# Optimization experiments

Hardware: AMD Instinct MI355X
Metric: run time of the kernel (lower is better)

The kernel has to match this reference:

```python
import jax, jax.numpy as jnp
import numpy as np

N = 50000
E = 1600000
IN_DIM = 128
H = 8
D = 16  # out_dim per head


def setup_inputs() -> dict:
    key = jax.random.key(0)
    ks = jax.random.split(key, 9)
    h = jax.random.normal(ks[0], (N, IN_DIM), dtype=jnp.float32)
    src = jax.random.randint(ks[1], (E,), 0, N, dtype=jnp.int32)
    dst = jax.random.randint(ks[2], (E,), 0, N, dtype=jnp.int32)
    s = 1.0 / np.sqrt(IN_DIM)
    WQ = jax.random.uniform(ks[3], (IN_DIM, H * D), jnp.float32, -s, s)
    WK = jax.random.uniform(ks[4], (IN_DIM, H * D), jnp.float32, -s, s)
    WV = jax.random.uniform(ks[5], (IN_DIM, H * D), jnp.float32, -s, s)
    bQ = jax.random.uniform(ks[6], (H * D,), jnp.float32, -s, s)
    bK = jax.random.uniform(ks[7], (H * D,), jnp.float32, -s, s)
    bV = jax.random.uniform(ks[8], (H * D,), jnp.float32, -s, s)
    return {"h": h, "src": src, "dst": dst, "WQ": WQ, "WK": WK, "WV": WV,
            "bQ": bQ, "bK": bK, "bV": bV}


def reference(h, src, dst, WQ, WK, WV, bQ, bK, bV):
    # Node projections -> [N, H, D]
    Q = (h @ WQ + bQ).reshape(-1, H, D)
    K = (h @ WK + bK).reshape(-1, H, D)
    V = (h @ WV + bV).reshape(-1, H, D)
    # Edge scores: dot(K[src], Q[dst]) per head, scaled+clamped exp -> [E, H]
    scale = jnp.float32(np.sqrt(D))
    score = jnp.exp(jnp.clip(jnp.sum(K[src] * Q[dst], axis=-1) / scale, -5.0, 5.0))
    # Scatter-sum to destination nodes
    wV = jax.ops.segment_sum(score[:, :, None] * V[src], dst, num_segments=N)  # [N, H, D]
    z = jax.ops.segment_sum(score, dst, num_segments=N)  # [N, H]
    return wV / z[:, :, None]
```

## Files before the change

kernel.cpp:

```cpp
#include <hip/hip_runtime.h>

#define N_NODES 50000
#define N_PAD   50048
#define N_EDGES 1600000
#define HD 128
#define CHUNK 4096
#define NCHUNK ((N_EDGES + CHUNK - 1) / CHUNK)
#define NBUCKET ((N_NODES + 127) / 128)

typedef __attribute__((ext_vector_type(8))) short short8;
typedef __attribute__((ext_vector_type(4))) float floatx4;

union U4S8 { uint4 u; short8 s; };

__device__ __forceinline__ unsigned short f2bf(float f) {
    unsigned u = __float_as_uint(f);
    unsigned r = (u + 0x7fffu + ((u >> 16) & 1u)) >> 16;
    return (unsigned short)r;
}

__global__ __launch_bounds__(256) void k_chunkhist(
    const int* __restrict__ dst, int* __restrict__ chunkhist, int* __restrict__ btot,
    const float* __restrict__ WQ, const float* __restrict__ WK, const float* __restrict__ WV,
    unsigned short* __restrict__ Wf) {
    int t = threadIdx.x, c = blockIdx.x;
    if (c >= NCHUNK) {
        int tid = (c - NCHUNK) * 256 + t;
        int lane = tid & 63;
        int kstep = (tid >> 6) & 3;
        int ntile = tid >> 8;
        int g = ntile >> 3;
        int col = (ntile & 7) * 16 + (lane & 15);
        int k0 = kstep * 32 + (lane >> 4) * 8;
        const float* W = (g == 0) ? WQ : (g == 1) ? WK : WV;
        unsigned short r[8];
#pragma unroll
        for (int j = 0; j < 8; ++j)
            r[j] = f2bf(W[(size_t)(k0 + j) * HD + col]);
        *(uint4*)(Wf + (size_t)tid * 8) = *(uint4*)r;
        return;
    }
    __shared__ int hist[NBUCKET];
    for (int i = t; i < NBUCKET; i += 256) hist[i] = 0;
    __syncthreads();
    int e0 = c * CHUNK;
    int cnt = min(CHUNK, N_EDGES - e0);
    const uint4* d4 = (const uint4*)(dst + e0);
    int cnt4 = cnt >> 2;
    for (int i = t; i < cnt4; i += 256) {
        uint4 v = d4[i];
        atomicAdd(&hist[v.x >> 7], 1);
        atomicAdd(&hist[v.y >> 7], 1);
        atomicAdd(&hist[v.z >> 7], 1);
        atomicAdd(&hist[v.w >> 7], 1);
    }
    __syncthreads();
    for (int i = t; i < NBUCKET; i += 256) {
        int v = hist[i];
        chunkhist[c * NBUCKET + i] = v;
        if (v) atomicAdd(&btot[i], v);
    }
}

__global__ __launch_bounds__(256) void k_choff(const int* __restrict__ chunkhist,
                                               const int* __restrict__ btot,
                                               int* __restrict__ bucket_ptr,
                                               int* __restrict__ chunkoff) {
    int b = blockIdx.x, t = threadIdx.x;
    int x = 0;
    for (int i = t; i < NBUCKET; i += 256)
        if (i < b) x += btot[i];
    __shared__ int red[256];
    red[t] = x;
    __syncthreads();
    for (int off = 128; off > 0; off >>= 1) {
        if (t < off) red[t] += red[t + off];
        __syncthreads();
    }
    int base = red[0];
    if (t == 0) {
        bucket_ptr[b] = base;
        if (b == NBUCKET - 1) bucket_ptr[NBUCKET] = base + btot[b];
    }
    const int PER = (NCHUNK + 255) / 256;
    int c0 = t * PER;
    int v[PER];
    int s = 0;
#pragma unroll
    for (int i = 0; i < PER; ++i) {
        int c = c0 + i;
        v[i] = (c < NCHUNK) ? chunkhist[c * NBUCKET + b] : 0;
        s += v[i];
    }
    __shared__ int part[256];
    part[t] = s;
    __syncthreads();
    for (int off = 1; off < 256; off <<= 1) {
        int y = (t >= off) ? part[t - off] : 0;
        __syncthreads();
        part[t] += y;
        __syncthreads();
    }
    int run = base + part[t] - s;
#pragma unroll
    for (int i = 0; i < PER; ++i) {
        int c = c0 + i;
        if (c < NCHUNK) { chunkoff[c * NBUCKET + b] = run; run += v[i]; }
    }
}

__global__ __launch_bounds__(256) void k_scatter(const int* __restrict__ src,
                                                 const int* __restrict__ dst,
                                                 const int* __restrict__ chunkoff,
                                                 int* __restrict__ packed) {
    __shared__ int cur[NBUCKET];
    int t = threadIdx.x, c = blockIdx.x;
    for (int i = t; i < NBUCKET; i += 256) cur[i] = chunkoff[c * NBUCKET + i];
    __syncthreads();
    int e0 = c * CHUNK;
    int cnt = min(CHUNK, N_EDGES - e0);
    const uint4* d4 = (const uint4*)(dst + e0);
    const uint4* s4 = (const uint4*)(src + e0);
    int cnt4 = cnt >> 2;
    for (int i = t; i < cnt4; i += 256) {
        uint4 d = d4[i];
        uint4 s = s4[i];
        int pos;
        pos = atomicAdd(&cur[d.x >> 7], 1); packed[pos] = (s.x << 7) | (d.x & 127);
        pos = atomicAdd(&cur[d.y >> 7], 1); packed[pos] = (s.y << 7) | (d.y & 127);
        pos = atomicAdd(&cur[d.z >> 7], 1); packed[pos] = (s.z << 7) | (d.z & 127);
        pos = atomicAdd(&cur[d.w >> 7], 1); packed[pos] = (s.w << 7) | (d.w & 127);
    }
}

__global__ __launch_bounds__(256) void k_finalize(const int* __restrict__ bucket_ptr,
                                                  const int* __restrict__ packed,
                                                  int* __restrict__ row_ptr,
                                                  int* __restrict__ col_src) {
    __shared__ int hist[128], part[128], cur[128];
    int b = blockIdx.x, t = threadIdx.x;
    if (t < 128) hist[t] = 0;
    __syncthreads();
    int ebeg = bucket_ptr[b], eend = bucket_ptr[b + 1];
    int m = eend - ebeg;
    for (int i = t; i < m; i += 256)
        atomicAdd(&hist[packed[ebeg + i] & 127], 1);
    __syncthreads();
    int v = 0;
    if (t < 128) { v = hist[t]; part[t] = v; }
    __syncthreads();
    for (int off = 1; off < 128; off <<= 1) {
        int x = 0;
        if (t < 128 && t >= off) x = part[t - off];
        __syncthreads();
        if (t < 128) part[t] += x;
        __syncthreads();
    }
    if (t < 128) {
        int excl = part[t] - v;
        int node = b * 128 + t;
        if (node < N_NODES) row_ptr[node] = ebeg + excl;
        if (node == N_NODES - 1) row_ptr[N_NODES] = eend;
        cur[t] = ebeg + excl;
    }
    __syncthreads();
    for (int i = t; i < m; i += 256) {
        int p = packed[ebeg + i];
        int pos = atomicAdd(&cur[p & 127], 1);
        col_src[pos] = p >> 7;
    }
}


__global__ __launch_bounds__(256) void proj_mfma(
    const float* __restrict__ h, const unsigned short* __restrict__ Wf,
    const float* __restrict__ bQ, const float* __restrict__ bK, const float* __restrict__ bV,
    float* __restrict__ Qo, unsigned short* __restrict__ Kb, unsigned short* __restrict__ Vb) {
    int t = threadIdx.x;
    int w = t >> 6;
    int l = t & 63;
    int row0 = blockIdx.x * 64 + w * 16;
    int arow = row0 + (l & 15);
    int akoff = (l >> 4) * 8;
    bool rowok = arow < N_NODES;

    short8 a[4];
#pragma unroll
    for (int ks = 0; ks < 4; ++ks) {
        unsigned short r[8];
        if (rowok) {
            const float4* ap = (const float4*)(h + (size_t)arow * HD + ks * 32 + akoff);
            float4 f0 = ap[0], f1 = ap[1];
            r[0] = f2bf(f0.x); r[1] = f2bf(f0.y); r[2] = f2bf(f0.z); r[3] = f2bf(f0.w);
            r[4] = f2bf(f1.x); r[5] = f2bf(f1.y); r[6] = f2bf(f1.z); r[7] = f2bf(f1.w);
        } else {
#pragma unroll
            for (int j = 0; j < 8; ++j) r[j] = 0;
        }
        a[ks] = *(short8*)r;
    }

    int orow0 = row0 + (l >> 4) * 4;
#pragma unroll
    for (int nt = 0; nt < 24; ++nt) {
        floatx4 acc = (floatx4){0.f, 0.f, 0.f, 0.f};
#pragma unroll
        for (int ks = 0; ks < 4; ++ks) {
            U4S8 u;
            u.u = *(const uint4*)(Wf + ((size_t)(nt * 4 + ks) * 64 + l) * 8);
            acc = __builtin_amdgcn_mfma_f32_16x16x32_bf16(a[ks], u.s, acc, 0, 0, 0);
        }
        int g = nt >> 3;
        int cc = (nt & 7) * 16 + (l & 15);
        float bias = (g == 0) ? bQ[cc] : (g == 1) ? bK[cc] : bV[cc];
#pragma unroll
        for (int r = 0; r < 4; ++r) {
            int grow = orow0 + r;
            if (grow < N_NODES) {
                float val = acc[r] + bias;
                if (g == 0)      Qo[(size_t)grow * HD + cc] = val;
                else if (g == 1) Kb[(size_t)grow * HD + cc] = f2bf(val);
                else             Vb[(size_t)grow * HD + cc] = f2bf(val);
            }
        }
    }
}


__device__ __forceinline__ float blo(unsigned u) { return __uint_as_float(u << 16); }
__device__ __forceinline__ float bhi(unsigned u) { return __uint_as_float(u & 0xffff0000u); }

__global__ __launch_bounds__(256) void attn_kernel(
    const float* __restrict__ Q,
    const unsigned short* __restrict__ Kb, const unsigned short* __restrict__ Vb,
    const int* __restrict__ row_ptr, const int* __restrict__ col_src,
    float* __restrict__ out, int nbase, int nend) {
    int n = nbase + blockIdx.x * 4 + (threadIdx.x >> 6);
    if (n >= nend) return;
    int l = threadIdx.x & 63;
    int o = l >> 3;
    int p = l & 7;

    const float4* Qv = (const float4*)(Q + (size_t)n * HD + p * 16);
    float4 q0 = Qv[0], q1 = Qv[1], q2 = Qv[2], q3 = Qv[3];

    float acc[16];
#pragma unroll
    for (int j = 0; j < 16; ++j) acc[j] = 0.f;
    float z = 0.f;

    int beg = row_ptr[n], end = row_ptr[n + 1];

    for (int base = beg; base < end; base += 64) {
        int mm = min(64, end - base);
        int e_l = col_src[(base + l < end) ? (base + l) : beg];
        int steps = (mm + 7) >> 3;

        int s0 = __shfl(e_l, o);
        const uint4* Kp = (const uint4*)(Kb + (size_t)s0 * HD + p * 16);
        const uint4* Vp = (const uint4*)(Vb + (size_t)s0 * HD + p * 16);
        uint4 ka = Kp[0], kb = Kp[1], va = Vp[0], vb = Vp[1];

        for (int i = 0; i < steps; ++i) {
            uint4 nka = ka, nkb = kb, nva = va, nvb = vb;
            if (i + 1 < steps) {
                int s1 = __shfl(e_l, 8 * (i + 1) + o);
                const uint4* Kn = (const uint4*)(Kb + (size_t)s1 * HD + p * 16);
                const uint4* Vn = (const uint4*)(Vb + (size_t)s1 * HD + p * 16);
                nka = Kn[0]; nkb = Kn[1]; nva = Vn[0]; nvb = Vn[1];
            }
            float dot = blo(ka.x) * q0.x + bhi(ka.x) * q0.y
                      + blo(ka.y) * q0.z + bhi(ka.y) * q0.w
                      + blo(ka.z) * q1.x + bhi(ka.z) * q1.y
                      + blo(ka.w) * q1.z + bhi(ka.w) * q1.w
                      + blo(kb.x) * q2.x + bhi(kb.x) * q2.y
                      + blo(kb.y) * q2.z + bhi(kb.y) * q2.w
                      + blo(kb.z) * q3.x + bhi(kb.z) * q3.y
                      + blo(kb.w) * q3.z + bhi(kb.w) * q3.w;
            float sc = __expf(fminf(fmaxf(dot * 0.25f, -5.f), 5.f));
            if (8 * i + o >= mm) sc = 0.f;
            acc[0]  = fmaf(sc, blo(va.x), acc[0]);
            acc[1]  = fmaf(sc, bhi(va.x), acc[1]);
            acc[2]  = fmaf(sc, blo(va.y), acc[2]);
            acc[3]  = fmaf(sc, bhi(va.y), acc[3]);
            acc[4]  = fmaf(sc, blo(va.z), acc[4]);
            acc[5]  = fmaf(sc, bhi(va.z), acc[5]);
            acc[6]  = fmaf(sc, blo(va.w), acc[6]);
            acc[7]  = fmaf(sc, bhi(va.w), acc[7]);
            acc[8]  = fmaf(sc, blo(vb.x), acc[8]);
            acc[9]  = fmaf(sc, bhi(vb.x), acc[9]);
            acc[10] = fmaf(sc, blo(vb.y), acc[10]);
            acc[11] = fmaf(sc, bhi(vb.y), acc[11]);
            acc[12] = fmaf(sc, blo(vb.z), acc[12]);
            acc[13] = fmaf(sc, bhi(vb.z), acc[13]);
            acc[14] = fmaf(sc, blo(vb.w), acc[14]);
            acc[15] = fmaf(sc, bhi(vb.w), acc[15]);
            z += sc;
            ka = nka; kb = nkb; va = nva; vb = nvb;
        }
    }

#pragma unroll
    for (int j = 0; j < 16; ++j) {
        acc[j] += __shfl_xor(acc[j], 8);
        acc[j] += __shfl_xor(acc[j], 16);
        acc[j] += __shfl_xor(acc[j], 32);
    }
    z += __shfl_xor(z, 8);
    z += __shfl_xor(z, 16);
    z += __shfl_xor(z, 32);

    if (o == 0) {
        float inv = 1.f / z;
        float4* O = (float4*)(out + (size_t)n * HD + p * 16);
        O[0] = (float4){acc[0] * inv,  acc[1] * inv,  acc[2] * inv,  acc[3] * inv};
        O[1] = (float4){acc[4] * inv,  acc[5] * inv,  acc[6] * inv,  acc[7] * inv};
        O[2] = (float4){acc[8] * inv,  acc[9] * inv,  acc[10] * inv, acc[11] * inv};
        O[3] = (float4){acc[12] * inv, acc[13] * inv, acc[14] * inv, acc[15] * inv};
    }
}


static inline char* align256(char* p) {
    return (char*)(((uintptr_t)p + 255) & ~(uintptr_t)255);
}

extern "C" void kernel_launch(void* const* d_in, const int* in_sizes, int n_in,
                              void* d_out, int out_size, void* d_ws, size_t ws_size,
                              hipStream_t stream) {
    const float* h  = (const float*)d_in[0];
    const int*   src = (const int*)d_in[1];
    const int*   dst = (const int*)d_in[2];
    const float* WQ = (const float*)d_in[3];
    const float* WK = (const float*)d_in[4];
    const float* WV = (const float*)d_in[5];
    const float* bQ = (const float*)d_in[6];
    const float* bK = (const float*)d_in[7];
    const float* bV = (const float*)d_in[8];
    float* out = (float*)d_out;

    char* p = (char*)d_ws;
    float* Q = (float*)p;                    p += (size_t)N_PAD * HD * 4;
    unsigned short* Kb = (unsigned short*)p; p += (size_t)N_PAD * HD * 2;
    unsigned short* Vb = (unsigned short*)p; p += (size_t)N_PAD * HD * 2;
    unsigned short* Wf = (unsigned short*)p; p += (size_t)24 * 4 * 64 * 8 * 2;
    p = align256(p);
    int* row_ptr    = (int*)p;               p += (N_NODES + 2) * 4;
    p = align256(p);
    int* bucket_ptr = (int*)p;               p += (NBUCKET + 1) * 4;
    p = align256(p);
    int* btot       = (int*)p;               p += NBUCKET * 4;
    p = align256(p);
    int* chunkhist  = (int*)p;               p += (size_t)NCHUNK * NBUCKET * 4;
    p = align256(p);
    int* chunkoff   = (int*)p;               p += (size_t)NCHUNK * NBUCKET * 4;
    p = align256(p);
    int* packed     = (int*)p;               p += (size_t)N_EDGES * 4;
    p = align256(p);
    int* col_src    = (int*)p;               p += (size_t)N_EDGES * 4;

    (void)hipMemsetAsync(btot, 0, NBUCKET * sizeof(int), stream);
    k_chunkhist<<<NCHUNK + 24, 256, 0, stream>>>(dst, chunkhist, btot, WQ, WK, WV, Wf);
    k_choff<<<NBUCKET, 256, 0, stream>>>(chunkhist, btot, bucket_ptr, chunkoff);
    k_scatter<<<NCHUNK, 256, 0, stream>>>(src, dst, chunkoff, packed);
    k_finalize<<<NBUCKET, 256, 0, stream>>>(bucket_ptr, packed, row_ptr, col_src);
    proj_mfma<<<N_PAD / 64, 256, 0, stream>>>(h, Wf, bQ, bK, bV, Q, Kb, Vb);
    const int T1 = 16668, T2 = 33336;
    attn_kernel<<<(T1 + 3) / 4, 256, 0, stream>>>(Q, Kb, Vb, row_ptr, col_src, out, 0, T1);
    attn_kernel<<<(T2 - T1 + 3) / 4, 256, 0, stream>>>(Q, Kb, Vb, row_ptr, col_src, out, T1, T2);
    attn_kernel<<<(N_NODES - T2 + 3) / 4, 256, 0, stream>>>(Q, Kb, Vb, row_ptr, col_src, out, T2, N_NODES);
}
```

Measured before the change: 273.2 us.

## Fuse projection into scatter kernel, deepen attention gather pipeline, single attn launch

The MFMA node projection now runs as extra blocks of the scatter kernel, so the two independent phases share one launch and overlap. The attention kernel loads 16 edges per step into double-buffered registers instead of prefetching one edge ahead, which puts more gathers in flight. The three split attention launches become one, with launch_bounds set to a minimum of 4 blocks. The wider buffers raise register pressure, and mixing scatter and projection blocks in one grid could unbalance the schedule.

```diff
diff --git a/kernel.cpp b/kernel.cpp
--- a/kernel.cpp
+++ b/kernel.cpp
@@ -7,6 +7,7 @@
 #define CHUNK 4096
 #define NCHUNK ((N_EDGES + CHUNK - 1) / CHUNK)
 #define NBUCKET ((N_NODES + 127) / 128)
+#define PROJ_BLOCKS (N_PAD / 64)
 
 typedef __attribute__((ext_vector_type(8))) short short8;
 typedef __attribute__((ext_vector_type(4))) float floatx4;
@@ -109,12 +110,66 @@
     }
 }
 
-__global__ __launch_bounds__(256) void k_scatter(const int* __restrict__ src,
-                                                 const int* __restrict__ dst,
-                                                 const int* __restrict__ chunkoff,
-                                                 int* __restrict__ packed) {
+__global__ __launch_bounds__(256) void k_scatter_proj(
+    const int* __restrict__ src, const int* __restrict__ dst,
+    const int* __restrict__ chunkoff, int* __restrict__ packed,
+    const float* __restrict__ h, const unsigned short* __restrict__ Wf,
+    const float* __restrict__ bQ, const float* __restrict__ bK, const float* __restrict__ bV,
+    float* __restrict__ Qo, unsigned short* __restrict__ Kb, unsigned short* __restrict__ Vb) {
+    int c = blockIdx.x;
+    int t = threadIdx.x;
+    if (c >= NCHUNK) {
+        int blk = c - NCHUNK;
+        int w = t >> 6;
+        int l = t & 63;
+        int row0 = blk * 64 + w * 16;
+        int arow = row0 + (l & 15);
+        int akoff = (l >> 4) * 8;
+        bool rowok = arow < N_NODES;
+
+        short8 a[4];
+#pragma unroll
+        for (int ks = 0; ks < 4; ++ks) {
+            unsigned short r[8];
+            if (rowok) {
+                const float4* ap = (const float4*)(h + (size_t)arow * HD + ks * 32 + akoff);
+                float4 f0 = ap[0], f1 = ap[1];
+                r[0] = f2bf(f0.x); r[1] = f2bf(f0.y); r[2] = f2bf(f0.z); r[3] = f2bf(f0.w);
+                r[4] = f2bf(f1.x); r[5] = f2bf(f1.y); r[6] = f2bf(f1.z); r[7] = f2bf(f1.w);
+            } else {
+#pragma unroll
+                for (int j = 0; j < 8; ++j) r[j] = 0;
+            }
+            a[ks] = *(short8*)r;
+        }
+
+        int orow0 = row0 + (l >> 4) * 4;
+#pragma unroll
+        for (int nt = 0; nt < 24; ++nt) {
+            floatx4 acc = (floatx4){0.f, 0.f, 0.f, 0.f};
+#pragma unroll
+            for (int ks = 0; ks < 4; ++ks) {
+                U4S8 u;
+                u.u = *(const uint4*)(Wf + ((size_t)(nt * 4 + ks) * 64 + l) * 8);
+                acc = __builtin_amdgcn_mfma_f32_16x16x32_bf16(a[ks], u.s, acc, 0, 0, 0);
+            }
+            int g = nt >> 3;
+            int cc = (nt & 7) * 16 + (l & 15);
+            float bias = (g == 0) ? bQ[cc] : (g == 1) ? bK[cc] : bV[cc];
+#pragma unroll
+            for (int r = 0; r < 4; ++r) {
+                int grow = orow0 + r;
+                if (grow < N_NODES) {
+                    float val = acc[r] + bias;
+                    if (g == 0)      Qo[(size_t)grow * HD + cc] = val;
+                    else if (g == 1) Kb[(size_t)grow * HD + cc] = f2bf(val);
+                    else             Vb[(size_t)grow * HD + cc] = f2bf(val);
+                }
+            }
+        }
+        return;
+    }
     __shared__ int cur[NBUCKET];
-    int t = threadIdx.x, c = blockIdx.x;
     for (int i = t; i < NBUCKET; i += 256) cur[i] = chunkoff[c * NBUCKET + i];
     __syncthreads();
     int e0 = c * CHUNK;
@@ -172,71 +227,59 @@
 }
 
 
-__global__ __launch_bounds__(256) void proj_mfma(
-    const float* __restrict__ h, const unsigned short* __restrict__ Wf,
-    const float* __restrict__ bQ, const float* __restrict__ bK, const float* __restrict__ bV,
-    float* __restrict__ Qo, unsigned short* __restrict__ Kb, unsigned short* __restrict__ Vb) {
-    int t = threadIdx.x;
-    int w = t >> 6;
-    int l = t & 63;
-    int row0 = blockIdx.x * 64 + w * 16;
-    int arow = row0 + (l & 15);
-    int akoff = (l >> 4) * 8;
-    bool rowok = arow < N_NODES;
-
-    short8 a[4];
-#pragma unroll
-    for (int ks = 0; ks < 4; ++ks) {
-        unsigned short r[8];
-        if (rowok) {
-            const float4* ap = (const float4*)(h + (size_t)arow * HD + ks * 32 + akoff);
-            float4 f0 = ap[0], f1 = ap[1];
-            r[0] = f2bf(f0.x); r[1] = f2bf(f0.y); r[2] = f2bf(f0.z); r[3] = f2bf(f0.w);
-            r[4] = f2bf(f1.x); r[5] = f2bf(f1.y); r[6] = f2bf(f1.z); r[7] = f2bf(f1.w);
-        } else {
-#pragma unroll
-            for (int j = 0; j < 8; ++j) r[j] = 0;
-        }
-        a[ks] = *(short8*)r;
-    }
-
-    int orow0 = row0 + (l >> 4) * 4;
-#pragma unroll
-    for (int nt = 0; nt < 24; ++nt) {
-        floatx4 acc = (floatx4){0.f, 0.f, 0.f, 0.f};
-#pragma unroll
-        for (int ks = 0; ks < 4; ++ks) {
-            U4S8 u;
-            u.u = *(const uint4*)(Wf + ((size_t)(nt * 4 + ks) * 64 + l) * 8);
-            acc = __builtin_amdgcn_mfma_f32_16x16x32_bf16(a[ks], u.s, acc, 0, 0, 0);
-        }
-        int g = nt >> 3;
-        int cc = (nt & 7) * 16 + (l & 15);
-        float bias = (g == 0) ? bQ[cc] : (g == 1) ? bK[cc] : bV[cc];
-#pragma unroll
-        for (int r = 0; r < 4; ++r) {
-            int grow = orow0 + r;
-            if (grow < N_NODES) {
-                float val = acc[r] + bias;
-                if (g == 0)      Qo[(size_t)grow * HD + cc] = val;
-                else if (g == 1) Kb[(size_t)grow * HD + cc] = f2bf(val);
-                else             Vb[(size_t)grow * HD + cc] = f2bf(val);
-            }
-        }
-    }
-}
-
-
 __device__ __forceinline__ float blo(unsigned u) { return __uint_as_float(u << 16); }
 __device__ __forceinline__ float bhi(unsigned u) { return __uint_as_float(u & 0xffff0000u); }
 
-__global__ __launch_bounds__(256) void attn_kernel(
+#define LOADE(slot, K0, K1, V0, V1)                                           \
+    {                                                                         \
+        int _s = __shfl(e_l, (slot));                                         \
+        if ((slot) < mm) {                                                    \
+            const uint4* _Kp = (const uint4*)(Kb + (size_t)_s * HD + p * 16); \
+            const uint4* _Vp = (const uint4*)(Vb + (size_t)_s * HD + p * 16); \
+            K0 = _Kp[0]; K1 = _Kp[1]; V0 = _Vp[0]; V1 = _Vp[1];               \
+        } else {                                                              \
+            K0 = Z; K1 = Z; V0 = Z; V1 = Z;                                   \
+        }                                                                     \
+    }
+
+#define EDGE(KA, KB, VA, VB, slot)                                            \
+    {                                                                         \
+        float dot = blo(KA.x) * q0.x + bhi(KA.x) * q0.y                       \
+                  + blo(KA.y) * q0.z + bhi(KA.y) * q0.w                       \
+                  + blo(KA.z) * q1.x + bhi(KA.z) * q1.y                       \
+                  + blo(KA.w) * q1.z + bhi(KA.w) * q1.w                       \
+                  + blo(KB.x) * q2.x + bhi(KB.x) * q2.y                       \
+                  + blo(KB.y) * q2.z + bhi(KB.y) * q2.w                       \
+                  + blo(KB.z) * q3.x + bhi(KB.z) * q3.y                       \
+                  + blo(KB.w) * q3.z + bhi(KB.w) * q3.w;                      \
+        float sc = __expf(fminf(fmaxf(dot * 0.25f, -5.f), 5.f));              \
+        if ((slot) >= mm) sc = 0.f;                                           \
+        acc[0]  = fmaf(sc, blo(VA.x), acc[0]);                                \
+        acc[1]  = fmaf(sc, bhi(VA.x), acc[1]);                                \
+        acc[2]  = fmaf(sc, blo(VA.y), acc[2]);                                \
+        acc[3]  = fmaf(sc, bhi(VA.y), acc[3]);                                \
+        acc[4]  = fmaf(sc, blo(VA.z), acc[4]);                                \
+        acc[5]  = fmaf(sc, bhi(VA.z), acc[5]);                                \
+        acc[6]  = fmaf(sc, blo(VA.w), acc[6]);                                \
+        acc[7]  = fmaf(sc, bhi(VA.w), acc[7]);                                \
+        acc[8]  = fmaf(sc, blo(VB.x), acc[8]);                                \
+        acc[9]  = fmaf(sc, bhi(VB.x), acc[9]);                                \
+        acc[10] = fmaf(sc, blo(VB.y), acc[10]);                               \
+        acc[11] = fmaf(sc, bhi(VB.y), acc[11]);                               \
+        acc[12] = fmaf(sc, blo(VB.z), acc[12]);                               \
+        acc[13] = fmaf(sc, bhi(VB.z), acc[13]);                               \
+        acc[14] = fmaf(sc, blo(VB.w), acc[14]);                               \
+        acc[15] = fmaf(sc, bhi(VB.w), acc[15]);                               \
+        z += sc;                                                              \
+    }
+
+__global__ __launch_bounds__(256, 4) void attn_kernel(
     const float* __restrict__ Q,
     const unsigned short* __restrict__ Kb, const unsigned short* __restrict__ Vb,
     const int* __restrict__ row_ptr, const int* __restrict__ col_src,
-    float* __restrict__ out, int nbase, int nend) {
-    int n = nbase + blockIdx.x * 4 + (threadIdx.x >> 6);
-    if (n >= nend) return;
+    float* __restrict__ out) {
+    int n = blockIdx.x * 4 + (threadIdx.x >> 6);
+    if (n >= N_NODES) return;
     int l = threadIdx.x & 63;
     int o = l >> 3;
     int p = l & 7;
@@ -250,53 +293,41 @@
     float z = 0.f;
 
     int beg = row_ptr[n], end = row_ptr[n + 1];
+    const uint4 Z = {0u, 0u, 0u, 0u};
 
     for (int base = beg; base < end; base += 64) {
         int mm = min(64, end - base);
         int e_l = col_src[(base + l < end) ? (base + l) : beg];
-        int steps = (mm + 7) >> 3;
-
-        int s0 = __shfl(e_l, o);
-        const uint4* Kp = (const uint4*)(Kb + (size_t)s0 * HD + p * 16);
-        const uint4* Vp = (const uint4*)(Vb + (size_t)s0 * HD + p * 16);
-        uint4 ka = Kp[0], kb = Kp[1], va = Vp[0], vb = Vp[1];
-
-        for (int i = 0; i < steps; ++i) {
-            uint4 nka = ka, nkb = kb, nva = va, nvb = vb;
-            if (i + 1 < steps) {
-                int s1 = __shfl(e_l, 8 * (i + 1) + o);
-                const uint4* Kn = (const uint4*)(Kb + (size_t)s1 * HD + p * 16);
-                const uint4* Vn = (const uint4*)(Vb + (size_t)s1 * HD + p * 16);
-                nka = Kn[0]; nkb = Kn[1]; nva = Vn[0]; nvb = Vn[1];
+        int steps = (mm + 15) >> 4;
+
+        uint4 kA0, kA1, vA0, vA1, kB0, kB1, vB0, vB1;
+        uint4 kC0, kC1, vC0, vC1, kD0, kD1, vD0, vD1;
+
+        LOADE(o, kA0, kA1, vA0, vA1);
+        LOADE(8 + o, kB0, kB1, vB0, vB1);
+
+        int i = 0;
+        while (true) {
+            bool has1 = (i + 1 < steps);
+            if (has1) {
+                int b1 = 16 * (i + 1);
+                LOADE(b1 + o, kC0, kC1, vC0, vC1);
+                LOADE(b1 + 8 + o, kD0, kD1, vD0, vD1);
             }
-            float dot = blo(ka.x) * q0.x + bhi(ka.x) * q0.y
-                      + blo(ka.y) * q0.z + bhi(ka.y) * q0.w
-                      + blo(ka.z) * q1.x + bhi(ka.z) * q1.y
-                      + blo(ka.w) * q1.z + bhi(ka.w) * q1.w
-                      + blo(kb.x) * q2.x + bhi(kb.x) * q2.y
-                      + blo(kb.y) * q2.z + bhi(kb.y) * q2.w
-                      + blo(kb.z) * q3.x + bhi(kb.z) * q3.y
-                      + blo(kb.w) * q3.z + bhi(kb.w) * q3.w;
-            float sc = __expf(fminf(fmaxf(dot * 0.25f, -5.f), 5.f));
-            if (8 * i + o >= mm) sc = 0.f;
-            acc[0]  = fmaf(sc, blo(va.x), acc[0]);
-            acc[1]  = fmaf(sc, bhi(va.x), acc[1]);
-            acc[2]  = fmaf(sc, blo(va.y), acc[2]);
-            acc[3]  = fmaf(sc, bhi(va.y), acc[3]);
-            acc[4]  = fmaf(sc, blo(va.z), acc[4]);
-            acc[5]  = fmaf(sc, bhi(va.z), acc[5]);
-            acc[6]  = fmaf(sc, blo(va.w), acc[6]);
-            acc[7]  = fmaf(sc, bhi(va.w), acc[7]);
-            acc[8]  = fmaf(sc, blo(vb.x), acc[8]);
-            acc[9]  = fmaf(sc, bhi(vb.x), acc[9]);
-            acc[10] = fmaf(sc, blo(vb.y), acc[10]);
-            acc[11] = fmaf(sc, bhi(vb.y), acc[11]);
-            acc[12] = fmaf(sc, blo(vb.z), acc[12]);
-            acc[13] = fmaf(sc, bhi(vb.z), acc[13]);
-            acc[14] = fmaf(sc, blo(vb.w), acc[14]);
-            acc[15] = fmaf(sc, bhi(vb.w), acc[15]);
-            z += sc;
-            ka = nka; kb = nkb; va = nva; vb = nvb;
+            int b0 = 16 * i;
+            EDGE(kA0, kA1, vA0, vA1, b0 + o);
+            EDGE(kB0, kB1, vB0, vB1, b0 + 8 + o);
+            if (!has1) break;
+            if (i + 2 < steps) {
+                int b2 = 16 * (i + 2);
+                LOADE(b2 + o, kA0, kA1, vA0, vA1);
+                LOADE(b2 + 8 + o, kB0, kB1, vB0, vB1);
+            }
+            int b1 = 16 * (i + 1);
+            EDGE(kC0, kC1, vC0, vC1, b1 + o);
+            EDGE(kD0, kD1, vD0, vD1, b1 + 8 + o);
+            i += 2;
+            if (i >= steps) break;
         }
     }
 
@@ -362,11 +393,8 @@
     (void)hipMemsetAsync(btot, 0, NBUCKET * sizeof(int), stream);
     k_chunkhist<<<NCHUNK + 24, 256, 0, stream>>>(dst, chunkhist, btot, WQ, WK, WV, Wf);
     k_choff<<<NBUCKET, 256, 0, stream>>>(chunkhist, btot, bucket_ptr, chunkoff);
-    k_scatter<<<NCHUNK, 256, 0, stream>>>(src, dst, chunkoff, packed);
+    k_scatter_proj<<<NCHUNK + PROJ_BLOCKS, 256, 0, stream>>>(
+        src, dst, chunkoff, packed, h, Wf, bQ, bK, bV, Q, Kb, Vb);
     k_finalize<<<NBUCKET, 256, 0, stream>>>(bucket_ptr, packed, row_ptr, col_src);
-    proj_mfma<<<N_PAD / 64, 256, 0, stream>>>(h, Wf, bQ, bK, bV, Q, Kb, Vb);
-    const int T1 = 16668, T2 = 33336;
-    attn_kernel<<<(T1 + 3) / 4, 256, 0, stream>>>(Q, Kb, Vb, row_ptr, col_src, out, 0, T1);
-    attn_kernel<<<(T2 - T1 + 3) / 4, 256, 0, stream>>>(Q, Kb, Vb, row_ptr, col_src, out, T1, T2);
-    attn_kernel<<<(N_NODES - T2 + 3) / 4, 256, 0, stream>>>(Q, Kb, Vb, row_ptr, col_src, out, T2, N_NODES);
-}
+    attn_kernel<<<(N_NODES + 3) / 4, 256, 0, stream>>>(Q, Kb, Vb, row_ptr, col_src, out);
+}
```

Result: slower. 330.2 us (+20.9%).

## Fuse projection into scatter kernel and merge attention launches into one

Applied to the files above, without the earlier changes.

Runs the MFMA Q/K/V projection blocks as extra blocks of the edge scatter kernel, so projection overlaps with the scatter and one launch is removed. Also replaces the three split attention launches with a single launch over all nodes. This cuts launch overhead and the idle tails between kernels, at the cost of a larger mixed-work grid whose block scheduling may be less even.

```diff
diff --git a/kernel.cpp b/kernel.cpp
--- a/kernel.cpp
+++ b/kernel.cpp
@@ -7,6 +7,7 @@
 #define CHUNK 4096
 #define NCHUNK ((N_EDGES + CHUNK - 1) / CHUNK)
 #define NBUCKET ((N_NODES + 127) / 128)
+#define PROJ_BLOCKS (N_PAD / 64)
 
 typedef __attribute__((ext_vector_type(8))) short short8;
 typedef __attribute__((ext_vector_type(4))) float floatx4;
@@ -109,12 +110,66 @@
     }
 }
 
-__global__ __launch_bounds__(256) void k_scatter(const int* __restrict__ src,
-                                                 const int* __restrict__ dst,
-                                                 const int* __restrict__ chunkoff,
-                                                 int* __restrict__ packed) {
+__global__ __launch_bounds__(256) void k_scatter_proj(
+    const int* __restrict__ src, const int* __restrict__ dst,
+    const int* __restrict__ chunkoff, int* __restrict__ packed,
+    const float* __restrict__ h, const unsigned short* __restrict__ Wf,
+    const float* __restrict__ bQ, const float* __restrict__ bK, const float* __restrict__ bV,
+    float* __restrict__ Qo, unsigned short* __restrict__ Kb, unsigned short* __restrict__ Vb) {
+    int c = blockIdx.x;
+    int t = threadIdx.x;
+    if (c >= NCHUNK) {
+        int blk = c - NCHUNK;
+        int w = t >> 6;
+        int l = t & 63;
+        int row0 = blk * 64 + w * 16;
+        int arow = row0 + (l & 15);
+        int akoff = (l >> 4) * 8;
+        bool rowok = arow < N_NODES;
+
+        short8 a[4];
+#pragma unroll
+        for (int ks = 0; ks < 4; ++ks) {
+            unsigned short r[8];
+            if (rowok) {
+                const float4* ap = (const float4*)(h + (size_t)arow * HD + ks * 32 + akoff);
+                float4 f0 = ap[0], f1 = ap[1];
+                r[0] = f2bf(f0.x); r[1] = f2bf(f0.y); r[2] = f2bf(f0.z); r[3] = f2bf(f0.w);
+                r[4] = f2bf(f1.x); r[5] = f2bf(f1.y); r[6] = f2bf(f1.z); r[7] = f2bf(f1.w);
+            } else {
+#pragma unroll
+                for (int j = 0; j < 8; ++j) r[j] = 0;
+            }
+            a[ks] = *(short8*)r;
+        }
+
+        int orow0 = row0 + (l >> 4) * 4;
+#pragma unroll
+        for (int nt = 0; nt < 24; ++nt) {
+            floatx4 acc = (floatx4){0.f, 0.f, 0.f, 0.f};
+#pragma unroll
+            for (int ks = 0; ks < 4; ++ks) {
+                U4S8 u;
+                u.u = *(const uint4*)(Wf + ((size_t)(nt * 4 + ks) * 64 + l) * 8);
+                acc = __builtin_amdgcn_mfma_f32_16x16x32_bf16(a[ks], u.s, acc, 0, 0, 0);
+            }
+            int g = nt >> 3;
+            int cc = (nt & 7) * 16 + (l & 15);
+            float bias = (g == 0) ? bQ[cc] : (g == 1) ? bK[cc] : bV[cc];
+#pragma unroll
+            for (int r = 0; r < 4; ++r) {
+                int grow = orow0 + r;
+                if (grow < N_NODES) {
+                    float val = acc[r] + bias;
+                    if (g == 0)      Qo[(size_t)grow * HD + cc] = val;
+                    else if (g == 1) Kb[(size_t)grow * HD + cc] = f2bf(val);
+                    else             Vb[(size_t)grow * HD + cc] = f2bf(val);
+                }
+            }
+        }
+        return;
+    }
     __shared__ int cur[NBUCKET];
-    int t = threadIdx.x, c = blockIdx.x;
     for (int i = t; i < NBUCKET; i += 256) cur[i] = chunkoff[c * NBUCKET + i];
     __syncthreads();
     int e0 = c * CHUNK;
@@ -172,61 +227,6 @@
 }
 
 
-__global__ __launch_bounds__(256) void proj_mfma(
-    const float* __restrict__ h, const unsigned short* __restrict__ Wf,
-    const float* __restrict__ bQ, const float* __restrict__ bK, const float* __restrict__ bV,
-    float* __restrict__ Qo, unsigned short* __restrict__ Kb, unsigned short* __restrict__ Vb) {
-    int t = threadIdx.x;
-    int w = t >> 6;
-    int l = t & 63;
-    int row0 = blockIdx.x * 64 + w * 16;
-    int arow = row0 + (l & 15);
-    int akoff = (l >> 4) * 8;
-    bool rowok = arow < N_NODES;
-
-    short8 a[4];
-#pragma unroll
-    for (int ks = 0; ks < 4; ++ks) {
-        unsigned short r[8];
-        if (rowok) {
-            const float4* ap = (const float4*)(h + (size_t)arow * HD + ks * 32 + akoff);
-            float4 f0 = ap[0], f1 = ap[1];
-            r[0] = f2bf(f0.x); r[1] = f2bf(f0.y); r[2] = f2bf(f0.z); r[3] = f2bf(f0.w);
-            r[4] = f2bf(f1.x); r[5] = f2bf(f1.y); r[6] = f2bf(f1.z); r[7] = f2bf(f1.w);
-        } else {
-#pragma unroll
-            for (int j = 0; j < 8; ++j) r[j] = 0;
-        }
-        a[ks] = *(short8*)r;
-    }
-
-    int orow0 = row0 + (l >> 4) * 4;
-#pragma unroll
-    for (int nt = 0; nt < 24; ++nt) {
-        floatx4 acc = (floatx4){0.f, 0.f, 0.f, 0.f};
-#pragma unroll
-        for (int ks = 0; ks < 4; ++ks) {
-            U4S8 u;
-            u.u = *(const uint4*)(Wf + ((size_t)(nt * 4 + ks) * 64 + l) * 8);
-            acc = __builtin_amdgcn_mfma_f32_16x16x32_bf16(a[ks], u.s, acc, 0, 0, 0);
-        }
-        int g = nt >> 3;
-        int cc = (nt & 7) * 16 + (l & 15);
-        float bias = (g == 0) ? bQ[cc] : (g == 1) ? bK[cc] : bV[cc];
-#pragma unroll
-        for (int r = 0; r < 4; ++r) {
-            int grow = orow0 + r;
-            if (grow < N_NODES) {
-                float val = acc[r] + bias;
-                if (g == 0)      Qo[(size_t)grow * HD + cc] = val;
-                else if (g == 1) Kb[(size_t)grow * HD + cc] = f2bf(val);
-                else             Vb[(size_t)grow * HD + cc] = f2bf(val);
-            }
-        }
-    }
-}
-
-
 __device__ __forceinline__ float blo(unsigned u) { return __uint_as_float(u << 16); }
 __device__ __forceinline__ float bhi(unsigned u) { return __uint_as_float(u & 0xffff0000u); }
 
@@ -234,9 +234,9 @@
     const float* __restrict__ Q,
     const unsigned short* __restrict__ Kb, const unsigned short* __restrict__ Vb,
     const int* __restrict__ row_ptr, const int* __restrict__ col_src,
-    float* __restrict__ out, int nbase, int nend) {
-    int n = nbase + blockIdx.x * 4 + (threadIdx.x >> 6);
-    if (n >= nend) return;
+    float* __restrict__ out) {
+    int n = blockIdx.x * 4 + (threadIdx.x >> 6);
+    if (n >= N_NODES) return;
     int l = threadIdx.x & 63;
     int o = l >> 3;
     int p = l & 7;
@@ -362,11 +362,8 @@
     (void)hipMemsetAsync(btot, 0, NBUCKET * sizeof(int), stream);
     k_chunkhist<<<NCHUNK + 24, 256, 0, stream>>>(dst, chunkhist, btot, WQ, WK, WV, Wf);
     k_choff<<<NBUCKET, 256, 0, stream>>>(chunkhist, btot, bucket_ptr, chunkoff);
-    k_scatter<<<NCHUNK, 256, 0, stream>>>(src, dst, chunkoff, packed);
+    k_scatter_proj<<<NCHUNK + PROJ_BLOCKS, 256, 0, stream>>>(
+        src, dst, chunkoff, packed, h, Wf, bQ, bK, bV, Q, Kb, Vb);
     k_finalize<<<NBUCKET, 256, 0, stream>>>(bucket_ptr, packed, row_ptr, col_src);
-    proj_mfma<<<N_PAD / 64, 256, 0, stream>>>(h, Wf, bQ, bK, bV, Q, Kb, Vb);
-    const int T1 = 16668, T2 = 33336;
-    attn_kernel<<<(T1 + 3) / 4, 256, 0, stream>>>(Q, Kb, Vb, row_ptr, col_src, out, 0, T1);
-    attn_kernel<<<(T2 - T1 + 3) / 4, 256, 0, stream>>>(Q, Kb, Vb, row_ptr, col_src, out, T1, T2);
-    attn_kernel<<<(N_NODES - T2 + 3) / 4, 256, 0, stream>>>(Q, Kb, Vb, row_ptr, col_src, out, T2, N_NODES);
-}
+    attn_kernel<<<(N_NODES + 3) / 4, 256, 0, stream>>>(Q, Kb, Vb, row_ptr, col_src, out);
+}
```

Measured after the change: 264.2 us. 3.3% less time.
